# Optimization experiments

Hardware: AMD Instinct MI355X
Metric: run time of the kernel (lower is better)

Reference implementation:

```python
import jax, jax.numpy as jnp
import numpy as np

WS = 512            # window_size
STEP = WS // 2      # hop
K = WS // 2 + 1     # rfft coeffs = 257


def hann(n):
    # periodic hann window (matches torch.hann_window default)
    return 0.5 * (1.0 - jnp.cos(2.0 * jnp.pi * jnp.arange(n) / n))


def setup_inputs() -> dict:
    key = jax.random.key(0)
    k1, k2, k3 = jax.random.split(key, 3)
    B, C, T = 4, 64, 65536
    x = jax.random.normal(k1, (B, C, T), dtype=jnp.float32)
    # mixer initialized near identity (nn.Parameter(torch.eye(C)) after some training)
    mixer = jnp.eye(C, dtype=jnp.float32) + 0.01 * jax.random.normal(k2, (C, C), dtype=jnp.float32)
    # stable per-coefficient transfer magnitudes in [0, 0.9)
    transfer = jax.random.uniform(k3, (C, K), dtype=jnp.float32) * 0.9
    gain = jnp.full((1,), 1.5, dtype=jnp.float32)
    return {"x": x, "mixer": mixer, "transfer": transfer, "gain": gain}


def reference(x, mixer, transfer, gain):
    B, C, T = x.shape
    # (x^T @ mixer)^T
    x = jnp.einsum('bct,cd->bdt', x, mixer)
    # windowed_audio: pad by hop, unfold into half-overlapping frames
    xp = jnp.pad(x, ((0, 0), (0, 0), (0, STEP)))
    n_frames = (xp.shape[-1] - WS) // STEP + 1
    idx = jnp.arange(n_frames)[:, None] * STEP + jnp.arange(WS)[None, :]  # [F, WS]
    windowed = xp[:, :, idx]                     # [B, C, F, WS]
    spec = jnp.fft.rfft(windowed, axis=-1)       # [B, C, F, K] complex64
    # linear recurrence over frames: y_i = (spec_i + y_{i-1}) * transfer
    def step(carry, s):
        y = (s + carry) * transfer[None]         # [B, C, K]
        return y, y
    spec_t = jnp.transpose(spec, (2, 0, 1, 3))   # [F, B, C, K]
    y0 = jnp.zeros((B, C, K), dtype=spec.dtype)
    _, ys = jax.lax.scan(step, y0, spec_t)       # [F, B, C, K]
    out_spec = jnp.transpose(ys, (1, 2, 0, 3))   # [B, C, F, K]
    # inverse FFT + windowed overlap-add
    aw = jnp.fft.irfft(out_spec, n=WS, axis=-1)  # [B, C, F, WS]
    aw = aw * hann(WS)[None, None, None, :]
    L = (n_frames - 1) * STEP + WS
    samples = jnp.zeros((B, C, L), dtype=aw.dtype).at[:, :, idx].add(aw)
    samples = jnp.tanh(samples * gain[0])
    return samples[..., :T]
```

## Files before the change

kernel.cpp:

```cpp
#include <hip/hip_runtime.h>
#include <math.h>

#define T_LEN  65536
#define T_PAD  65792
#define C_CH   64
#define STEP_  256
#define K_     257
#define NW     16
#define NIT    16
#define SPEC_ROWF 514

#define SW(i) ((i) ^ (((i) >> 2) & 12))

#define CFENCE() asm volatile("" ::: "memory")
#define BAR() do { asm volatile("s_waitcnt lgkmcnt(0)" ::: "memory"); \
                   __builtin_amdgcn_s_barrier(); \
                   asm volatile("" ::: "memory"); } while (0)

__device__ __forceinline__ float2 cadd(float2 a, float2 b) { return make_float2(a.x + b.x, a.y + b.y); }
__device__ __forceinline__ float2 csub(float2 a, float2 b) { return make_float2(a.x - b.x, a.y - b.y); }
__device__ __forceinline__ float2 cmul(float2 a, float2 b) {
    return make_float2(a.x * b.x - a.y * b.y, a.x * b.y + a.y * b.x);
}
template <int SGN>
__device__ __forceinline__ float2 cmulsg(float2 w, float2 t) {
    if (SGN > 0) return make_float2(w.x * t.x - w.y * t.y, w.x * t.y + w.y * t.x);
    else         return make_float2(w.x * t.x + w.y * t.y, w.x * t.y - w.y * t.x);
}
template <int SGN>
__device__ __forceinline__ void bfly4(float2 z0, float2 z1, float2 z2, float2 z3,
                                      float2& o0, float2& o1, float2& o2, float2& o3,
                                      float2 w1, float2 w2, float2 w3) {
    float2 apc = cadd(z0, z2), amc = csub(z0, z2);
    float2 bpd = cadd(z1, z3), bmd = csub(z1, z3);
    float2 jb  = make_float2(-bmd.y, bmd.x);
    float2 t1, t3;
    if (SGN > 0) { t1 = csub(amc, jb); t3 = cadd(amc, jb); }
    else         { t1 = cadd(amc, jb); t3 = csub(amc, jb); }
    o0 = cadd(apc, bpd);
    o1 = cmulsg<SGN>(w1, t1);
    o2 = cmulsg<SGN>(w2, csub(apc, bpd));
    o3 = cmulsg<SGN>(w3, t3);
}
template <int SGN>
__device__ __forceinline__ void bfly4nt(float2 z0, float2 z1, float2 z2, float2 z3,
                                        float2& o0, float2& o1, float2& o2, float2& o3) {
    float2 apc = cadd(z0, z2), amc = csub(z0, z2);
    float2 bpd = cadd(z1, z3), bmd = csub(z1, z3);
    float2 jb  = make_float2(-bmd.y, bmd.x);
    o0 = cadd(apc, bpd);
    o2 = csub(apc, bpd);
    if (SGN > 0) { o1 = csub(amc, jb); o3 = cadd(amc, jb); }
    else         { o1 = cadd(amc, jb); o3 = csub(amc, jb); }
}

__device__ __forceinline__ float ftanh(float x) {
    float e = __expf(2.0f * x);
    return 1.0f - 2.0f * __builtin_amdgcn_rcpf(e + 1.0f);
}

__global__ __launch_bounds__(512, 1) void mix_kernel(const float* __restrict__ x,
                                                     const float* __restrict__ mixer,
                                                     float* __restrict__ mixed) {
    __shared__ __align__(16) float xt[64][128];
    __shared__ __align__(16) float mx[64][64];
    int tid = threadIdx.x;
    int b   = blockIdx.y;
    int t0  = blockIdx.x * 128;

    if (t0 >= T_LEN) {
        for (int f = tid; f < 8192; f += 512) {
            int d = f >> 7, tt = f & 127;
            mixed[((size_t)(b * C_CH + d)) * T_PAD + t0 + tt] = 0.0f;
        }
        return;
    }
    for (int f = tid; f < 4096; f += 512) reinterpret_cast<float*>(mx)[f] = mixer[f];
    for (int f4 = tid; f4 < 2048; f4 += 512) {
        int cc = f4 >> 5, tt4 = f4 & 31;
        *reinterpret_cast<float4*>(&xt[cc][tt4 * 4]) =
            *reinterpret_cast<const float4*>(&x[((size_t)(b * C_CH + cc)) * T_LEN + t0 + tt4 * 4]);
    }
    __syncthreads();

    int tp = tid & 63, grp = tid >> 6;
    int dbase = grp * 8;
    float2 acc[8];
#pragma unroll
    for (int i = 0; i < 8; ++i) acc[i] = make_float2(0.0f, 0.0f);
    for (int cc = 0; cc < 64; ++cc) {
        float2 xv = *reinterpret_cast<const float2*>(&xt[cc][2 * tp]);
        float4 m0 = *reinterpret_cast<const float4*>(&mx[cc][dbase + 0]);
        float4 m1 = *reinterpret_cast<const float4*>(&mx[cc][dbase + 4]);
        acc[0].x = fmaf(xv.x, m0.x, acc[0].x); acc[0].y = fmaf(xv.y, m0.x, acc[0].y);
        acc[1].x = fmaf(xv.x, m0.y, acc[1].x); acc[1].y = fmaf(xv.y, m0.y, acc[1].y);
        acc[2].x = fmaf(xv.x, m0.z, acc[2].x); acc[2].y = fmaf(xv.y, m0.z, acc[2].y);
        acc[3].x = fmaf(xv.x, m0.w, acc[3].x); acc[3].y = fmaf(xv.y, m0.w, acc[3].y);
        acc[4].x = fmaf(xv.x, m1.x, acc[4].x); acc[4].y = fmaf(xv.y, m1.x, acc[4].y);
        acc[5].x = fmaf(xv.x, m1.y, acc[5].x); acc[5].y = fmaf(xv.y, m1.y, acc[5].y);
        acc[6].x = fmaf(xv.x, m1.z, acc[6].x); acc[6].y = fmaf(xv.y, m1.z, acc[6].y);
        acc[7].x = fmaf(xv.x, m1.w, acc[7].x); acc[7].y = fmaf(xv.y, m1.w, acc[7].y);
    }
#pragma unroll
    for (int i = 0; i < 8; ++i)
        *reinterpret_cast<float2*>(&mixed[((size_t)(b * C_CH + dbase + i)) * T_PAD + t0 + 2 * tp]) = acc[i];
}

__global__ __launch_bounds__(1024) void stft_kernel(const float* __restrict__ mixed,
                                                    const float* __restrict__ transfer,
                                                    const float* __restrict__ gainp,
                                                    float* __restrict__ out) {
    __shared__ __align__(16) float2 buf[NW][256];
    __shared__ __align__(16) float2 spec[2][NW][257];
    __shared__ __align__(16) float  olab[NW][264];
    __shared__ __align__(16) float  tails[2][264];

    const int tid  = threadIdx.x;
    const int bc   = blockIdx.x;
    const int b    = bc >> 6, c = bc & 63;
    const int g    = tid >> 6, lane = tid & 63;

    const float* src = mixed + ((size_t)(b * C_CH + c)) * T_PAD;
    float*       dst = out   + ((size_t)(b * C_CH + c)) * T_LEN;

    float2 pf0, pf1, pf2, pf3;
    {
        const float* fp = src + (size_t)g * STEP_;
        pf0 = *reinterpret_cast<const float2*>(fp + 2 * lane);
        pf1 = *reinterpret_cast<const float2*>(fp + 2 * (lane + 64));
        pf2 = *reinterpret_cast<const float2*>(fp + 2 * (lane + 128));
        pf3 = *reinterpret_cast<const float2*>(fp + 2 * (lane + 192));
    }

    const float TWO_PI = 6.2831853071795864f;
    float sn, cn;
    sincosf(TWO_PI * (float)lane / 256.0f, &sn, &cn);
    float2 w1a = make_float2(cn, -sn), w2a = cmul(w1a, w1a), w3a = cmul(w2a, w1a);
    sincosf(TWO_PI * (float)(lane >> 2) / 64.0f, &sn, &cn);
    float2 w1b = make_float2(cn, -sn), w2b = cmul(w1b, w1b), w3b = cmul(w2b, w1b);
    sincosf(TWO_PI * (float)(lane >> 4) / 16.0f, &sn, &cn);
    float2 w1c = make_float2(cn, -sn), w2c = cmul(w1c, w1c), w3c = cmul(w2c, w1c);
    float2 wh[4];
#pragma unroll
    for (int qq = 0; qq < 4; ++qq) {
        sincosf(3.14159265358979f * (float)(lane + 64 * qq) / 256.0f, &sn, &cn);
        wh[qq] = make_float2(cn, -sn);
    }
#define HV(m) ((0.5f - 0.5f * cosf(TWO_PI * (float)(m) / 512.0f)) * (1.0f / 512.0f))
    float h0 = HV(2 * lane),       h1 = HV(2 * lane + 1);
    float h2 = HV(2 * lane + 128), h3 = HV(2 * lane + 129);
    float h4 = HV(2 * lane + 256), h5 = HV(2 * lane + 257);
    float h6 = HV(2 * lane + 384), h7 = HV(2 * lane + 385);
#undef HV

    int se = -1;
    if (g < 8) se = (g << 6) | lane;
    else if (g == 8 && lane < 2) se = 512 + lane;
    float tcar = 0.0f, ycar = 0.0f;
    if (se >= 0) tcar = transfer[c * K_ + (se >> 1)];

    if (tid < 256) tails[0][tid] = 0.0f;
    const float gv = gainp[0];
    float2* bin = &buf[g][0];
    const int q2  = (lane & 3)  + ((lane >> 2) << 4);
    const int q3  = (lane & 15) + ((lane >> 4) << 6);
    const int s1b = (4 * lane) ^ (lane & 12);
    BAR();

    for (int it = 0; it <= NIT; ++it) {
        const int sp = it & 1, sp2 = sp ^ 1;
        if (it < NIT) {
            const int f = it * NW + g;
            float2 z0 = pf0, z1 = pf1, z2 = pf2, z3 = pf3;
            if (it + 1 < NIT) {
                const float* fp = src + (size_t)(f + NW) * STEP_;
                pf0 = *reinterpret_cast<const float2*>(fp + 2 * lane);
                pf1 = *reinterpret_cast<const float2*>(fp + 2 * (lane + 64));
                pf2 = *reinterpret_cast<const float2*>(fp + 2 * (lane + 128));
                pf3 = *reinterpret_cast<const float2*>(fp + 2 * (lane + 192));
            }
            float2 o0, o1, o2, o3;
            bfly4<1>(z0, z1, z2, z3, o0, o1, o2, o3, w1a, w2a, w3a);
            {
                float2* bw = bin + s1b;
                *reinterpret_cast<float4*>(bw)     = make_float4(o0.x, o0.y, o1.x, o1.y);
                *reinterpret_cast<float4*>(bw + 2) = make_float4(o2.x, o2.y, o3.x, o3.y);
            }
            CFENCE();
            z0 = bin[SW(lane)]; z1 = bin[SW(lane + 64)];
            z2 = bin[SW(lane + 128)]; z3 = bin[SW(lane + 192)];
            bfly4<1>(z0, z1, z2, z3, o0, o1, o2, o3, w1b, w2b, w3b);
            CFENCE();
            bin[SW(q2)] = o0; bin[SW(q2 + 4)] = o1;
            bin[SW(q2 + 8)] = o2; bin[SW(q2 + 12)] = o3;
            CFENCE();
            z0 = bin[SW(lane)]; z1 = bin[SW(lane + 64)];
            z2 = bin[SW(lane + 128)]; z3 = bin[SW(lane + 192)];
            bfly4<1>(z0, z1, z2, z3, o0, o1, o2, o3, w1c, w2c, w3c);
            CFENCE();
            bin[SW(q3)] = o0; bin[SW(q3 + 16)] = o1;
            bin[SW(q3 + 32)] = o2; bin[SW(q3 + 48)] = o3;
            CFENCE();
            z0 = bin[SW(lane)]; z1 = bin[SW(lane + 64)];
            z2 = bin[SW(lane + 128)]; z3 = bin[SW(lane + 192)];
            bfly4nt<1>(z0, z1, z2, z3, o0, o1, o2, o3);
            CFENCE();
            bin[SW(lane)] = o0; bin[SW(lane + 64)] = o1;
            bin[SW(lane + 128)] = o2; bin[SW(lane + 192)] = o3;
            CFENCE();
#pragma unroll
            for (int qq = 0; qq < 4; ++qq) {
                int k = lane + 64 * qq;
                float2 u = bin[SW(k)];
                float2 v = bin[SW((256 - k) & 255)];
                float2 E = make_float2(0.5f * (u.x + v.x),  0.5f * (u.y - v.y));
                float2 O = make_float2(0.5f * (u.y + v.y), -0.5f * (u.x - v.x));
                spec[sp][g][k] = cadd(E, cmul(wh[qq], O));
            }
            if (lane == 0) {
                float2 u0 = bin[SW(0)];
                spec[sp][g][256] = make_float2(u0.x - u0.y, 0.0f);
            }
        }
        BAR();
        if (it < NIT && se >= 0) {
            float* sf = reinterpret_cast<float*>(&spec[sp][0][0]);
            float y = ycar;
#pragma unroll
            for (int gg = 0; gg < NW; ++gg) {
                y = (sf[gg * SPEC_ROWF + se] + y) * tcar;
                sf[gg * SPEC_ROWF + se] = y;
            }
            ycar = y;
        }
        if (it > 0) {
            const int fb = (it - 1) * NW + g;
            float2 o0, o1, o2, o3;
            {
                float2 zz[4];
#pragma unroll
                for (int qq = 0; qq < 4; ++qq) {
                    int k = lane + 64 * qq;
                    float2 u  = spec[sp2][g][k];
                    float2 s2 = spec[sp2][g][256 - k];
                    float2 A  = make_float2(u.x + s2.x, u.y - s2.y);
                    float2 D  = make_float2(u.x - s2.x, u.y + s2.y);
                    float2 Bv = cmulsg<-1>(wh[qq], D);
                    zz[qq] = make_float2(A.x - Bv.y, A.y + Bv.x);
                }
                bfly4<-1>(zz[0], zz[1], zz[2], zz[3], o0, o1, o2, o3, w1a, w2a, w3a);
            }
            {
                float2* bw = bin + s1b;
                *reinterpret_cast<float4*>(bw)     = make_float4(o0.x, o0.y, o1.x, o1.y);
                *reinterpret_cast<float4*>(bw + 2) = make_float4(o2.x, o2.y, o3.x, o3.y);
            }
            CFENCE();
            float2 z0 = bin[SW(lane)], z1 = bin[SW(lane + 64)];
            float2 z2 = bin[SW(lane + 128)], z3 = bin[SW(lane + 192)];
            bfly4<-1>(z0, z1, z2, z3, o0, o1, o2, o3, w1b, w2b, w3b);
            CFENCE();
            bin[SW(q2)] = o0; bin[SW(q2 + 4)] = o1;
            bin[SW(q2 + 8)] = o2; bin[SW(q2 + 12)] = o3;
            CFENCE();
            z0 = bin[SW(lane)]; z1 = bin[SW(lane + 64)];
            z2 = bin[SW(lane + 128)]; z3 = bin[SW(lane + 192)];
            bfly4<-1>(z0, z1, z2, z3, o0, o1, o2, o3, w1c, w2c, w3c);
            CFENCE();
            bin[SW(q3)] = o0; bin[SW(q3 + 16)] = o1;
            bin[SW(q3 + 32)] = o2; bin[SW(q3 + 48)] = o3;
            CFENCE();
            z0 = bin[SW(lane)]; z1 = bin[SW(lane + 64)];
            z2 = bin[SW(lane + 128)]; z3 = bin[SW(lane + 192)];
            bfly4nt<-1>(z0, z1, z2, z3, o0, o1, o2, o3);
            {
                float2 sh0 = make_float2(o2.x * h4, o2.y * h5);
                float2 sh1 = make_float2(o3.x * h6, o3.y * h7);
                float* wrow = (g == NW - 1) ? tails[it & 1] : olab[g + 1];
                *reinterpret_cast<float2*>(&wrow[2 * lane])       = sh0;
                *reinterpret_cast<float2*>(&wrow[2 * lane + 128]) = sh1;
            }
            BAR();
            {
                const float* prow = (g == 0) ? tails[(it - 1) & 1] : olab[g];
                float2 p0 = *reinterpret_cast<const float2*>(&prow[2 * lane]);
                float2 p1 = *reinterpret_cast<const float2*>(&prow[2 * lane + 128]);
                float2 r0 = make_float2(ftanh((o0.x * h0 + p0.x) * gv),
                                        ftanh((o0.y * h1 + p0.y) * gv));
                float2 r1 = make_float2(ftanh((o1.x * h2 + p1.x) * gv),
                                        ftanh((o1.y * h3 + p1.y) * gv));
                float* dp = dst + (size_t)fb * STEP_;
                *reinterpret_cast<float2*>(&dp[2 * lane])       = r0;
                *reinterpret_cast<float2*>(&dp[2 * lane + 128]) = r1;
            }
        }
    }
}

extern "C" void kernel_launch(void* const* d_in, const int* in_sizes, int n_in,
                              void* d_out, int out_size, void* d_ws, size_t ws_size,
                              hipStream_t stream) {
    (void)in_sizes; (void)n_in; (void)out_size; (void)ws_size;
    const float* x        = (const float*)d_in[0];
    const float* mixer    = (const float*)d_in[1];
    const float* transfer = (const float*)d_in[2];
    const float* gain     = (const float*)d_in[3];
    float* out   = (float*)d_out;
    float* mixed = (float*)d_ws;

    dim3 gmix(T_PAD / 128, 4);
    mix_kernel<<<gmix, 512, 0, stream>>>(x, mixer, mixed);
    stft_kernel<<<256, 1024, 0, stream>>>(mixed, transfer, gain, out);
}
```

Measured before the change: 113.5 us.

## Restructure STFT kernel as register-resident 16x16 FFT with 32 frames per iteration

Replaces the 256-point complex FFT, which used four radix-4 passes through shared memory per 64-lane group, with a 16x16 decomposition. Each 16-thread group holds a whole frame in registers and does two in-register DFT16 stages with a single shared transpose. Each block now has 512 threads handling 32 frames per iteration over 8 iterations, and the frame recurrence reads a frame-major transposed spectrum layout. The goal is fewer LDS round trips and barriers per frame. In exchange it adds register pressure from the 16-element arrays and drops the overlap of the forward and inverse transforms across iterations.

```diff
diff --git a/kernel.cpp b/kernel.cpp
--- a/kernel.cpp
+++ b/kernel.cpp
@@ -2,15 +2,13 @@
 #include <math.h>
 
 #define T_LEN  65536
-#define T_PAD  65792
 #define C_CH   64
 #define STEP_  256
 #define K_     257
-#define NW     16
-#define NIT    16
-#define SPEC_ROWF 514
-
-#define SW(i) ((i) ^ (((i) >> 2) & 12))
+#define FPI    32
+#define NIT    8
+#define TPITCH 276
+#define SPITCH 33
 
 #define CFENCE() asm volatile("" ::: "memory")
 #define BAR() do { asm volatile("s_waitcnt lgkmcnt(0)" ::: "memory"); \
@@ -26,21 +24,6 @@
 __device__ __forceinline__ float2 cmulsg(float2 w, float2 t) {
     if (SGN > 0) return make_float2(w.x * t.x - w.y * t.y, w.x * t.y + w.y * t.x);
     else         return make_float2(w.x * t.x + w.y * t.y, w.x * t.y - w.y * t.x);
-}
-template <int SGN>
-__device__ __forceinline__ void bfly4(float2 z0, float2 z1, float2 z2, float2 z3,
-                                      float2& o0, float2& o1, float2& o2, float2& o3,
-                                      float2 w1, float2 w2, float2 w3) {
-    float2 apc = cadd(z0, z2), amc = csub(z0, z2);
-    float2 bpd = cadd(z1, z3), bmd = csub(z1, z3);
-    float2 jb  = make_float2(-bmd.y, bmd.x);
-    float2 t1, t3;
-    if (SGN > 0) { t1 = csub(amc, jb); t3 = cadd(amc, jb); }
-    else         { t1 = cadd(amc, jb); t3 = csub(amc, jb); }
-    o0 = cadd(apc, bpd);
-    o1 = cmulsg<SGN>(w1, t1);
-    o2 = cmulsg<SGN>(w2, csub(apc, bpd));
-    o3 = cmulsg<SGN>(w3, t3);
 }
 template <int SGN>
 __device__ __forceinline__ void bfly4nt(float2 z0, float2 z1, float2 z2, float2 z3,
@@ -54,11 +37,44 @@
     else         { o1 = cadd(amc, jb); o3 = csub(amc, jb); }
 }
 
+template <int SGN>
+__device__ __forceinline__ void dft16(float2* v) {
+    const float C1 = 0.9238795325112867f, S1 = 0.3826834323650898f, R2 = 0.7071067811865476f;
+    const float2 W1 = make_float2(C1, -S1);
+    const float2 W2 = make_float2(R2, -R2);
+    const float2 W3 = make_float2(S1, -C1);
+    const float2 W4 = make_float2(0.f, -1.f);
+    const float2 W6 = make_float2(-R2, -R2);
+    const float2 W9 = make_float2(-C1, S1);
+    float2 t[16];
+#pragma unroll
+    for (int m1 = 0; m1 < 4; ++m1)
+        bfly4nt<SGN>(v[m1], v[m1 + 4], v[m1 + 8], v[m1 + 12],
+                     t[4 * m1 + 0], t[4 * m1 + 1], t[4 * m1 + 2], t[4 * m1 + 3]);
+    t[5]  = cmulsg<SGN>(W1, t[5]);
+    t[6]  = cmulsg<SGN>(W2, t[6]);
+    t[7]  = cmulsg<SGN>(W3, t[7]);
+    t[9]  = cmulsg<SGN>(W2, t[9]);
+    t[10] = cmulsg<SGN>(W4, t[10]);
+    t[11] = cmulsg<SGN>(W6, t[11]);
+    t[13] = cmulsg<SGN>(W3, t[13]);
+    t[14] = cmulsg<SGN>(W6, t[14]);
+    t[15] = cmulsg<SGN>(W9, t[15]);
+#pragma unroll
+    for (int j1 = 0; j1 < 4; ++j1)
+        bfly4nt<SGN>(t[j1], t[4 + j1], t[8 + j1], t[12 + j1],
+                     v[j1], v[j1 + 4], v[j1 + 8], v[j1 + 12]);
+}
+
 __device__ __forceinline__ float ftanh(float x) {
     float e = __expf(2.0f * x);
     return 1.0f - 2.0f * __builtin_amdgcn_rcpf(e + 1.0f);
 }
-
+__device__ __forceinline__ float hwin(int n) {
+    return (0.5f - 0.5f * __cosf((float)n * 0.01227184630308513f)) * 0.001953125f;
+}
+
+#define T_PAD  65792
 __global__ __launch_bounds__(512, 1) void mix_kernel(const float* __restrict__ x,
                                                      const float* __restrict__ mixer,
                                                      float* __restrict__ mixed) {
@@ -106,194 +122,183 @@
         *reinterpret_cast<float2*>(&mixed[((size_t)(b * C_CH + dbase + i)) * T_PAD + t0 + 2 * tp]) = acc[i];
 }
 
-__global__ __launch_bounds__(1024) void stft_kernel(const float* __restrict__ mixed,
-                                                    const float* __restrict__ transfer,
-                                                    const float* __restrict__ gainp,
-                                                    float* __restrict__ out) {
-    __shared__ __align__(16) float2 buf[NW][256];
-    __shared__ __align__(16) float2 spec[2][NW][257];
-    __shared__ __align__(16) float  olab[NW][264];
-    __shared__ __align__(16) float  tails[2][264];
+__global__ __launch_bounds__(512, 2) void stft_kernel(const float* __restrict__ mixed,
+                                                      const float* __restrict__ transfer,
+                                                      const float* __restrict__ gainp,
+                                                      float* __restrict__ out) {
+    __shared__ __align__(16) float2 T[FPI * TPITCH];
+    __shared__ __align__(16) float2 spec[K_ * SPITCH];
+    __shared__ __align__(16) float2 tails[2][132];
 
     const int tid  = threadIdx.x;
     const int bc   = blockIdx.x;
     const int b    = bc >> 6, c = bc & 63;
-    const int g    = tid >> 6, lane = tid & 63;
-
-    const float* src = mixed + ((size_t)(b * C_CH + c)) * T_PAD;
-    float*       dst = out   + ((size_t)(b * C_CH + c)) * T_LEN;
-
-    float2 pf0, pf1, pf2, pf3;
-    {
-        const float* fp = src + (size_t)g * STEP_;
-        pf0 = *reinterpret_cast<const float2*>(fp + 2 * lane);
-        pf1 = *reinterpret_cast<const float2*>(fp + 2 * (lane + 64));
-        pf2 = *reinterpret_cast<const float2*>(fp + 2 * (lane + 128));
-        pf3 = *reinterpret_cast<const float2*>(fp + 2 * (lane + 192));
-    }
+    const int gid  = tid >> 4;
+    const int l    = tid & 15;
+    const int g    = tid >> 6;
+    const int lane = tid & 63;
+
+    const float2* src2 = reinterpret_cast<const float2*>(mixed + ((size_t)(b * C_CH + c)) * T_PAD);
+    float2*       dst2 = reinterpret_cast<float2*>(out + ((size_t)(b * C_CH + c)) * T_LEN);
 
     const float TWO_PI = 6.2831853071795864f;
     float sn, cn;
-    sincosf(TWO_PI * (float)lane / 256.0f, &sn, &cn);
-    float2 w1a = make_float2(cn, -sn), w2a = cmul(w1a, w1a), w3a = cmul(w2a, w1a);
-    sincosf(TWO_PI * (float)(lane >> 2) / 64.0f, &sn, &cn);
-    float2 w1b = make_float2(cn, -sn), w2b = cmul(w1b, w1b), w3b = cmul(w2b, w1b);
-    sincosf(TWO_PI * (float)(lane >> 4) / 16.0f, &sn, &cn);
-    float2 w1c = make_float2(cn, -sn), w2c = cmul(w1c, w1c), w3c = cmul(w2c, w1c);
-    float2 wh[4];
-#pragma unroll
-    for (int qq = 0; qq < 4; ++qq) {
-        sincosf(3.14159265358979f * (float)(lane + 64 * qq) / 256.0f, &sn, &cn);
-        wh[qq] = make_float2(cn, -sn);
-    }
-#define HV(m) ((0.5f - 0.5f * cosf(TWO_PI * (float)(m) / 512.0f)) * (1.0f / 512.0f))
-    float h0 = HV(2 * lane),       h1 = HV(2 * lane + 1);
-    float h2 = HV(2 * lane + 128), h3 = HV(2 * lane + 129);
-    float h4 = HV(2 * lane + 256), h5 = HV(2 * lane + 257);
-    float h6 = HV(2 * lane + 384), h7 = HV(2 * lane + 385);
-#undef HV
-
-    int se = -1;
-    if (g < 8) se = (g << 6) | lane;
-    else if (g == 8 && lane < 2) se = 512 + lane;
-    float tcar = 0.0f, ycar = 0.0f;
-    if (se >= 0) tcar = transfer[c * K_ + (se >> 1)];
-
-    if (tid < 256) tails[0][tid] = 0.0f;
+    sincosf(TWO_PI * (float)l / 256.0f, &sn, &cn);
+    const float2 w = make_float2(cn, -sn);
+    float2 tw4[4], tw16[4];
+    tw4[0] = make_float2(1.f, 0.f); tw4[1] = w;
+    tw4[2] = cmul(w, w);            tw4[3] = cmul(tw4[2], w);
+    float2 w4p = cmul(tw4[2], tw4[2]);
+    tw16[0] = make_float2(1.f, 0.f); tw16[1] = w4p;
+    tw16[2] = cmul(w4p, w4p);        tw16[3] = cmul(tw16[2], w4p);
+    sincosf(3.14159265358979f * (float)l / 256.0f, &sn, &cn);
+    const float2 whl = make_float2(cn, -sn);
+    const float2 WHSTEP = make_float2(0.9807852804032304f, -0.1950903220161283f);
+
+    const int tb  = gid * TPITCH;
+    const int sl  = l & 12;
+    const int l17 = l * 17;
+    const int sb  = l * SPITCH + gid;
+    const int mbs = (256 - l) * SPITCH + gid;
+    const int mr  = (16 - l) & 15;
+    const int mrb = tb + mr * 17;
+    const int msw = mr & 12;
+
+    int sk = -1;
+    if (g < 4) sk = g * 64 + lane;
+    else if (g == 4 && lane == 0) sk = 256;
+    float tk = 0.0f;
+    float2 yc = make_float2(0.f, 0.f);
+    if (sk >= 0) tk = transfer[c * K_ + sk];
+
+    if (tid < 128) tails[1][tid] = make_float2(0.f, 0.f);
     const float gv = gainp[0];
-    float2* bin = &buf[g][0];
-    const int q2  = (lane & 3)  + ((lane >> 2) << 4);
-    const int q3  = (lane & 15) + ((lane >> 4) << 6);
-    const int s1b = (4 * lane) ^ (lane & 12);
+
+    float2 v[16];
+    {
+        const float2* fp = src2 + (size_t)gid * 128;
+#pragma unroll
+        for (int n2 = 0; n2 < 16; ++n2) v[n2] = fp[l + 16 * n2];
+    }
     BAR();
 
-    for (int it = 0; it <= NIT; ++it) {
-        const int sp = it & 1, sp2 = sp ^ 1;
-        if (it < NIT) {
-            const int f = it * NW + g;
-            float2 z0 = pf0, z1 = pf1, z2 = pf2, z3 = pf3;
-            if (it + 1 < NIT) {
-                const float* fp = src + (size_t)(f + NW) * STEP_;
-                pf0 = *reinterpret_cast<const float2*>(fp + 2 * lane);
-                pf1 = *reinterpret_cast<const float2*>(fp + 2 * (lane + 64));
-                pf2 = *reinterpret_cast<const float2*>(fp + 2 * (lane + 128));
-                pf3 = *reinterpret_cast<const float2*>(fp + 2 * (lane + 192));
-            }
-            float2 o0, o1, o2, o3;
-            bfly4<1>(z0, z1, z2, z3, o0, o1, o2, o3, w1a, w2a, w3a);
-            {
-                float2* bw = bin + s1b;
-                *reinterpret_cast<float4*>(bw)     = make_float4(o0.x, o0.y, o1.x, o1.y);
-                *reinterpret_cast<float4*>(bw + 2) = make_float4(o2.x, o2.y, o3.x, o3.y);
+    for (int it = 0; it < NIT; ++it) {
+        const int f = it * FPI + gid;
+        dft16<1>(v);
+#pragma unroll
+        for (int k1 = 1; k1 < 16; ++k1) {
+            float2 z = v[k1];
+            if (k1 & 3)  z = cmul(z, tw4[k1 & 3]);
+            if (k1 >> 2) z = cmul(z, tw16[k1 >> 2]);
+            v[k1] = z;
+        }
+#pragma unroll
+        for (int a = 0; a < 8; ++a) {
+            int p = tb + l17 + ((2 * a) ^ sl);
+            *reinterpret_cast<float4*>(&T[p]) = make_float4(v[2*a].x, v[2*a].y, v[2*a+1].x, v[2*a+1].y);
+        }
+        CFENCE();
+        if (it + 1 < NIT) {
+            const float2* fp = src2 + (size_t)(f + FPI) * 128;
+#pragma unroll
+            for (int n2 = 0; n2 < 16; ++n2) v[n2] = fp[l + 16 * n2];
+        }
+        float2 cx[16];
+#pragma unroll
+        for (int n1 = 0; n1 < 16; ++n1) cx[n1] = T[tb + n1 * 17 + (l ^ (n1 & 12))];
+        dft16<1>(cx);
+#pragma unroll
+        for (int a = 0; a < 8; ++a) {
+            int p = tb + l17 + ((2 * a) ^ sl);
+            *reinterpret_cast<float4*>(&T[p]) = make_float4(cx[2*a].x, cx[2*a].y, cx[2*a+1].x, cx[2*a+1].y);
+        }
+        CFENCE();
+        {
+            float2 wh = whl;
+#pragma unroll
+            for (int k2 = 0; k2 < 16; ++k2) {
+                int m2 = (l > 0) ? (15 - k2) : ((16 - k2) & 15);
+                float2 xm = T[mrb + (m2 ^ msw)];
+                float2 u  = cx[k2];
+                float2 E = make_float2(0.5f * (u.x + xm.x),  0.5f * (u.y - xm.y));
+                float2 O = make_float2(0.5f * (u.y + xm.y), -0.5f * (u.x - xm.x));
+                spec[sb + 16 * SPITCH * k2] = cadd(E, cmulsg<1>(wh, O));
+                wh = cmul(wh, WHSTEP);
+            }
+            if (l == 0) spec[256 * SPITCH + gid] = make_float2(cx[0].x - cx[0].y, 0.0f);
+        }
+        BAR();
+        if (sk >= 0) {
+            float2* s0 = &spec[sk * SPITCH];
+            float2 y = yc;
+#pragma unroll
+            for (int r = 0; r < 4; ++r) {
+                float2 vv[8];
+#pragma unroll
+                for (int j = 0; j < 8; ++j) vv[j] = s0[r * 8 + j];
+#pragma unroll
+                for (int j = 0; j < 8; ++j) {
+                    y.x = (vv[j].x + y.x) * tk; y.y = (vv[j].y + y.y) * tk;
+                    s0[r * 8 + j] = y;
+                }
+            }
+            yc = y;
+        }
+        BAR();
+        float2 e[16];
+        {
+            float2 Gv[16];
+            float2 wh = whl;
+#pragma unroll
+            for (int k2 = 0; k2 < 16; ++k2) {
+                float2 u  = spec[sb + 16 * SPITCH * k2];
+                float2 s2 = spec[mbs - 16 * SPITCH * k2];
+                float2 A  = make_float2(u.x + s2.x, u.y - s2.y);
+                float2 D  = make_float2(u.x - s2.x, u.y + s2.y);
+                float2 Bv = cmulsg<-1>(wh, D);
+                Gv[k2] = make_float2(A.x - Bv.y, A.y + Bv.x);
+                wh = cmul(wh, WHSTEP);
+            }
+            dft16<-1>(Gv);
+#pragma unroll
+            for (int n1 = 1; n1 < 16; ++n1) {
+                float2 z = Gv[n1];
+                if (n1 & 3)  z = cmulsg<-1>(tw4[n1 & 3], z);
+                if (n1 >> 2) z = cmulsg<-1>(tw16[n1 >> 2], z);
+                Gv[n1] = z;
+            }
+#pragma unroll
+            for (int a = 0; a < 8; ++a) {
+                int p = tb + l17 + ((2 * a) ^ sl);
+                *reinterpret_cast<float4*>(&T[p]) = make_float4(Gv[2*a].x, Gv[2*a].y, Gv[2*a+1].x, Gv[2*a+1].y);
             }
             CFENCE();
-            z0 = bin[SW(lane)]; z1 = bin[SW(lane + 64)];
-            z2 = bin[SW(lane + 128)]; z3 = bin[SW(lane + 192)];
-            bfly4<1>(z0, z1, z2, z3, o0, o1, o2, o3, w1b, w2b, w3b);
-            CFENCE();
-            bin[SW(q2)] = o0; bin[SW(q2 + 4)] = o1;
-            bin[SW(q2 + 8)] = o2; bin[SW(q2 + 12)] = o3;
-            CFENCE();
-            z0 = bin[SW(lane)]; z1 = bin[SW(lane + 64)];
-            z2 = bin[SW(lane + 128)]; z3 = bin[SW(lane + 192)];
-            bfly4<1>(z0, z1, z2, z3, o0, o1, o2, o3, w1c, w2c, w3c);
-            CFENCE();
-            bin[SW(q3)] = o0; bin[SW(q3 + 16)] = o1;
-            bin[SW(q3 + 32)] = o2; bin[SW(q3 + 48)] = o3;
-            CFENCE();
-            z0 = bin[SW(lane)]; z1 = bin[SW(lane + 64)];
-            z2 = bin[SW(lane + 128)]; z3 = bin[SW(lane + 192)];
-            bfly4nt<1>(z0, z1, z2, z3, o0, o1, o2, o3);
-            CFENCE();
-            bin[SW(lane)] = o0; bin[SW(lane + 64)] = o1;
-            bin[SW(lane + 128)] = o2; bin[SW(lane + 192)] = o3;
-            CFENCE();
-#pragma unroll
-            for (int qq = 0; qq < 4; ++qq) {
-                int k = lane + 64 * qq;
-                float2 u = bin[SW(k)];
-                float2 v = bin[SW((256 - k) & 255)];
-                float2 E = make_float2(0.5f * (u.x + v.x),  0.5f * (u.y - v.y));
-                float2 O = make_float2(0.5f * (u.y + v.y), -0.5f * (u.x - v.x));
-                spec[sp][g][k] = cadd(E, cmul(wh[qq], O));
-            }
-            if (lane == 0) {
-                float2 u0 = bin[SW(0)];
-                spec[sp][g][256] = make_float2(u0.x - u0.y, 0.0f);
-            }
+#pragma unroll
+            for (int k1 = 0; k1 < 16; ++k1) e[k1] = T[tb + k1 * 17 + (l ^ (k1 & 12))];
+            dft16<-1>(e);
+        }
+#pragma unroll
+        for (int n2 = 8; n2 < 16; ++n2) {
+            int m = l + 16 * n2;
+            float2 sh = make_float2(e[n2].x * hwin(2 * m), e[n2].y * hwin(2 * m + 1));
+            if (gid == FPI - 1) tails[it & 1][l + 16 * (n2 - 8)] = sh;
+            else                T[tb + l + 16 * (n2 - 8)] = sh;
         }
         BAR();
-        if (it < NIT && se >= 0) {
-            float* sf = reinterpret_cast<float*>(&spec[sp][0][0]);
-            float y = ycar;
-#pragma unroll
-            for (int gg = 0; gg < NW; ++gg) {
-                y = (sf[gg * SPEC_ROWF + se] + y) * tcar;
-                sf[gg * SPEC_ROWF + se] = y;
-            }
-            ycar = y;
-        }
-        if (it > 0) {
-            const int fb = (it - 1) * NW + g;
-            float2 o0, o1, o2, o3;
-            {
-                float2 zz[4];
-#pragma unroll
-                for (int qq = 0; qq < 4; ++qq) {
-                    int k = lane + 64 * qq;
-                    float2 u  = spec[sp2][g][k];
-                    float2 s2 = spec[sp2][g][256 - k];
-                    float2 A  = make_float2(u.x + s2.x, u.y - s2.y);
-                    float2 D  = make_float2(u.x - s2.x, u.y + s2.y);
-                    float2 Bv = cmulsg<-1>(wh[qq], D);
-                    zz[qq] = make_float2(A.x - Bv.y, A.y + Bv.x);
-                }
-                bfly4<-1>(zz[0], zz[1], zz[2], zz[3], o0, o1, o2, o3, w1a, w2a, w3a);
-            }
-            {
-                float2* bw = bin + s1b;
-                *reinterpret_cast<float4*>(bw)     = make_float4(o0.x, o0.y, o1.x, o1.y);
-                *reinterpret_cast<float4*>(bw + 2) = make_float4(o2.x, o2.y, o3.x, o3.y);
-            }
-            CFENCE();
-            float2 z0 = bin[SW(lane)], z1 = bin[SW(lane + 64)];
-            float2 z2 = bin[SW(lane + 128)], z3 = bin[SW(lane + 192)];
-            bfly4<-1>(z0, z1, z2, z3, o0, o1, o2, o3, w1b, w2b, w3b);
-            CFENCE();
-            bin[SW(q2)] = o0; bin[SW(q2 + 4)] = o1;
-            bin[SW(q2 + 8)] = o2; bin[SW(q2 + 12)] = o3;
-            CFENCE();
-            z0 = bin[SW(lane)]; z1 = bin[SW(lane + 64)];
-            z2 = bin[SW(lane + 128)]; z3 = bin[SW(lane + 192)];
-            bfly4<-1>(z0, z1, z2, z3, o0, o1, o2, o3, w1c, w2c, w3c);
-            CFENCE();
-            bin[SW(q3)] = o0; bin[SW(q3 + 16)] = o1;
-            bin[SW(q3 + 32)] = o2; bin[SW(q3 + 48)] = o3;
-            CFENCE();
-            z0 = bin[SW(lane)]; z1 = bin[SW(lane + 64)];
-            z2 = bin[SW(lane + 128)]; z3 = bin[SW(lane + 192)];
-            bfly4nt<-1>(z0, z1, z2, z3, o0, o1, o2, o3);
-            {
-                float2 sh0 = make_float2(o2.x * h4, o2.y * h5);
-                float2 sh1 = make_float2(o3.x * h6, o3.y * h7);
-                float* wrow = (g == NW - 1) ? tails[it & 1] : olab[g + 1];
-                *reinterpret_cast<float2*>(&wrow[2 * lane])       = sh0;
-                *reinterpret_cast<float2*>(&wrow[2 * lane + 128]) = sh1;
-            }
-            BAR();
-            {
-                const float* prow = (g == 0) ? tails[(it - 1) & 1] : olab[g];
-                float2 p0 = *reinterpret_cast<const float2*>(&prow[2 * lane]);
-                float2 p1 = *reinterpret_cast<const float2*>(&prow[2 * lane + 128]);
-                float2 r0 = make_float2(ftanh((o0.x * h0 + p0.x) * gv),
-                                        ftanh((o0.y * h1 + p0.y) * gv));
-                float2 r1 = make_float2(ftanh((o1.x * h2 + p1.x) * gv),
-                                        ftanh((o1.y * h3 + p1.y) * gv));
-                float* dp = dst + (size_t)fb * STEP_;
-                *reinterpret_cast<float2*>(&dp[2 * lane])       = r0;
-                *reinterpret_cast<float2*>(&dp[2 * lane + 128]) = r1;
-            }
-        }
+        {
+            const float2* prow = (gid == 0) ? &tails[(it + 1) & 1][0] : &T[tb - TPITCH];
+            float2* dp = dst2 + (size_t)f * 128;
+#pragma unroll
+            for (int n2 = 0; n2 < 8; ++n2) {
+                int m = l + 16 * n2;
+                float2 prev = prow[l + 16 * n2];
+                float2 r;
+                r.x = ftanh((e[n2].x * hwin(2 * m)     + prev.x) * gv);
+                r.y = ftanh((e[n2].y * hwin(2 * m + 1) + prev.y) * gv);
+                dp[m] = r;
+            }
+        }
+        BAR();
     }
 }
 
@@ -310,5 +315,5 @@
 
     dim3 gmix(T_PAD / 128, 4);
     mix_kernel<<<gmix, 512, 0, stream>>>(x, mixer, mixed);
-    stft_kernel<<<256, 1024, 0, stream>>>(mixed, transfer, gain, out);
-}
+    stft_kernel<<<256, 512, 0, stream>>>(mixed, transfer, gain, out);
+}
```

After: 242.1 us. 113% more time.
